# Optimization experiments

Hardware: AMD Instinct MI355X
Metric: run time of the kernel (lower is better)

The kernel has to match this reference:

```python
import jax, jax.numpy as jnp
import numpy as np

K, N, D, NCONV, E = 3, 30000, 128, 6, 480000


def _graph_conv(x, src, dst, ew, Wp, bp, Wrel, Wroot):
    # SAGE-style project=True: pre-project+relu source features
    h = jax.nn.relu(x @ Wp + bp)                    # [N, D]
    msg = ew[:, None] * h[src]                      # [E, D] gather
    agg = jax.ops.segment_sum(msg, dst, num_segments=N)
    cnt = jax.ops.segment_sum(jnp.ones_like(ew), dst, num_segments=N)
    agg = agg / jnp.maximum(cnt, 1.0)[:, None]      # mean aggregation
    return agg @ Wrel + x @ Wroot                   # GraphConv: lin_rel(agg)+lin_root(x), bias=False


def setup_inputs() -> dict:
    key = jax.random.key(0)
    ks = jax.random.split(key, 16)
    w = lambda k, s: (jax.random.normal(k, s, jnp.float32) * 0.05)
    inp = {
        "H_K_prev": jax.random.normal(ks[0], (K, N, D), jnp.float32),
        "edgelists": jax.random.randint(ks[1], (K, 2, E), 0, N, jnp.int32),
        "spec_weight": jax.random.uniform(ks[2], (K, NCONV, E), jnp.float32),
        # 6 stacked GraphConv params
        "Wp": w(ks[3], (NCONV, D, D)),
        "bp": jnp.zeros((NCONV, D), jnp.float32),
        "Wrel": w(ks[4], (NCONV, D, D)),
        "Wroot": w(ks[5], (NCONV, D, D)),
        # combine projection (7D -> 3D) and proj_linear (4D -> D)
        "W_comb": w(ks[6], ((NCONV + 1) * D, 3 * D)),
        "b_comb": jnp.zeros((3 * D,), jnp.float32),
        "W_pl": w(ks[7], (4 * D, D)),
        "b_pl": jnp.zeros((D,), jnp.float32),
        # LSTM (torch gate order i,f,g,o)
        "Wih": w(ks[8], (4 * D, D)),
        "Whh": w(ks[9], (4 * D, D)),
        "bih": jnp.zeros((4 * D,), jnp.float32),
        "bhh": jnp.zeros((4 * D,), jnp.float32),
    }
    return inp


def reference(H_K_prev, edgelists, spec_weight, Wp, bp, Wrel, Wroot,
              W_comb, b_comb, W_pl, b_pl, Wih, Whh, bih, bhh):
    outs = []
    for k in range(K):  # fixed small history loop
        Hk = H_K_prev[k]
        src, dst = edgelists[k, 0], edgelists[k, 1]
        feats = [Hk] + [
            _graph_conv(Hk, src, dst, spec_weight[k, i],
                        Wp[i], bp[i], Wrel[i], Wroot[i])
            for i in range(NCONV)
        ]
        cat = jnp.concatenate(feats, axis=1)               # [N, 7D]
        proj = jax.nn.relu(cat @ W_comb + b_comb)          # [N, 3D] (dropout=eval identity)
        outs.append(jnp.concatenate([Hk, proj], axis=1) @ W_pl + b_pl)  # [N, D]
    xs = jnp.stack(outs, 0)                                # [K, N, D] time-major

    def cell(carry, x_t):
        h, c = carry
        gates = x_t @ Wih.T + h @ Whh.T + bih + bhh        # [N, 4D]
        i, f, g, o = jnp.split(gates, 4, axis=1)
        c = jax.nn.sigmoid(f) * c + jax.nn.sigmoid(i) * jnp.tanh(g)
        h = jax.nn.sigmoid(o) * jnp.tanh(c)
        return (h, c), None

    z = jnp.zeros((N, D), xs.dtype)
    (h, _), _ = jax.lax.scan(cell, (z, z), xs)
    return jax.nn.relu(h)[None]                            # [1, N, D]
```

## Files before the change

### kernel.cpp

```cpp
#include <hip/hip_runtime.h>
#include <math.h>

constexpr int NN  = 30000;
constexpr int DIM = 128;
constexpr int KH  = 3;
constexpr int NC  = 6;
constexpr int EE  = 480000;
constexpr int NBLK3 = (3 * NN + 255) / 256;

typedef __attribute__((ext_vector_type(8))) short short8;
typedef __attribute__((ext_vector_type(4))) float f32x4;
typedef __attribute__((ext_vector_type(2))) float f32x2;

__device__ __forceinline__ unsigned short f2bf(float f) {
    union { float f; unsigned int i; } c; c.f = f;
    unsigned int u = c.i;
    return (unsigned short)((u + 0x7fffu + ((u >> 16) & 1u)) >> 16);
}
__device__ __forceinline__ float bf2f(unsigned int u) {
    union { unsigned int i; float f; } c; c.i = u << 16; return c.f;
}
__device__ __forceinline__ unsigned int packbf(float x, float y) {
    return (unsigned int)f2bf(x) | ((unsigned int)f2bf(y) << 16);
}
__device__ __forceinline__ float fsig(float x) {
    return __builtin_amdgcn_rcpf(1.f + __expf(-x));
}
__device__ __forceinline__ float ftanh(float x) {
    return 2.f * fsig(2.f * x) - 1.f;
}

template<int OUT, bool RELU>
__global__ __launch_bounds__(256) void mgemm(
    const unsigned short* __restrict__ A1, int lda1,
    const unsigned short* __restrict__ A2, int lda2, int ksplit,
    const unsigned short* __restrict__ Bt, int ldb,
    const float* __restrict__ bias,
    void* __restrict__ Cv, int ldc,
    int M, int K, int nx)
{
    __shared__ __align__(16) unsigned char smem[2 * 128 * 80];
    unsigned char* As = smem;
    unsigned char* Bs = smem + 128 * 80;

    const int nwg  = gridDim.x;
    const int orig = blockIdx.x;
    const int q = nwg >> 3, r = nwg & 7;
    const int xcd = orig & 7, idx = orig >> 3;
    const int lin = (xcd < r ? xcd * (q + 1) : r * (q + 1) + (xcd - r) * q) + idx;
    const int bx = lin % nx, by = lin / nx;

    const int tid  = threadIdx.x;
    const int lane = tid & 63;
    const int w    = tid >> 6;
    const int wm   = w >> 1, wn = w & 1;
    const int lm   = lane & 15, lg = lane >> 4;
    const int bm   = by * 128;
    const int bn   = bx * 128;

    const int srow  = tid >> 1;
    const int shalf = tid & 1;

    f32x4 acc[4][4] = {};

    int arow = bm + srow; if (arow > M - 1) arow = M - 1;
    const int brow = bn + srow;

    for (int k0 = 0; k0 < K; k0 += 32) {
        const unsigned short* Ap; int la; int kk;
        if (k0 < ksplit) { Ap = A1; la = lda1; kk = k0; }
        else             { Ap = A2; la = lda2; kk = k0 - ksplit; }
        const float4* ga = (const float4*)(Ap + (size_t)arow * la + kk + shalf * 16);
        float4 a0 = ga[0], a1 = ga[1];
        const float4* gb = (const float4*)(Bt + (size_t)brow * ldb + k0 + shalf * 16);
        float4 b0 = gb[0], b1 = gb[1];

        __syncthreads();
        *(float4*)(As + srow * 80 + shalf * 32)      = a0;
        *(float4*)(As + srow * 80 + shalf * 32 + 16) = a1;
        *(float4*)(Bs + srow * 80 + shalf * 32)      = b0;
        *(float4*)(Bs + srow * 80 + shalf * 32 + 16) = b1;
        __syncthreads();

        short8 av[4], bv[4];
        #pragma unroll
        for (int f = 0; f < 4; ++f) {
            av[f] = *(const short8*)(As + (wm * 64 + f * 16 + lm) * 80 + lg * 16);
            bv[f] = *(const short8*)(Bs + (wn * 64 + f * 16 + lm) * 80 + lg * 16);
        }
        #pragma unroll
        for (int i = 0; i < 4; ++i)
            #pragma unroll
            for (int j = 0; j < 4; ++j)
                acc[i][j] = __builtin_amdgcn_mfma_f32_16x16x32_bf16(
                    av[i], bv[j], acc[i][j], 0, 0, 0);
    }

    #pragma unroll
    for (int i = 0; i < 4; ++i) {
        int row0 = bm + wm * 64 + i * 16 + lg * 4;
        #pragma unroll
        for (int j = 0; j < 4; ++j) {
            int col = bn + wn * 64 + j * 16 + lm;
            float bb = bias[col];
            #pragma unroll
            for (int r = 0; r < 4; ++r) {
                int row = row0 + r;
                if (row < M) {
                    float v = acc[i][j][r] + bb;
                    if (RELU) v = fmaxf(v, 0.f);
                    if (OUT == 0) {
                        ((unsigned short*)Cv)[(size_t)row * ldc + col] = f2bf(v);
                    } else {
                        unsigned int pk = __builtin_amdgcn_cvt_pk_fp8_f32(v, v, 0, false);
                        ((unsigned char*)Cv)[(size_t)row * ldc + col] = (unsigned char)pk;
                    }
                }
            }
        }
    }
}

__global__ void hist3(const int* __restrict__ EL, int* __restrict__ cnt)
{
    int i = blockIdx.x * 256 + threadIdx.x;
    if (i >= 3 * EE) return;
    int g = i / EE;
    int e = i - g * EE;
    int dst = EL[(size_t)g * 2 * EE + EE + e];
    atomicAdd(&cnt[g * NN + dst], 1);
}

__global__ __launch_bounds__(256) void scan_part(const int* __restrict__ cnt,
                                                 int* __restrict__ off,
                                                 int* __restrict__ bsum, int n)
{
    int lane = threadIdx.x & 63, wid = threadIdx.x >> 6;
    int i = blockIdx.x * 256 + threadIdx.x;
    int v = (i < n) ? cnt[i] : 0;
    int x = v;
    #pragma unroll
    for (int ofs = 1; ofs < 64; ofs <<= 1) {
        int t = __shfl_up(x, ofs, 64);
        if (lane >= ofs) x += t;
    }
    __shared__ int ws[4];
    if (lane == 63) ws[wid] = x;
    __syncthreads();
    int wo = 0;
    for (int j = 0; j < wid; ++j) wo += ws[j];
    if (i < n) off[i] = wo + x - v;
    if (threadIdx.x == 255) bsum[blockIdx.x] = wo + x;
}

__global__ __launch_bounds__(512) void scan_tops(const int* __restrict__ bsum,
                                                 int* __restrict__ btop, int nb)
{
    __shared__ int buf[512];
    int v = (threadIdx.x < nb) ? bsum[threadIdx.x] : 0;
    buf[threadIdx.x] = v;
    __syncthreads();
    #pragma unroll
    for (int ofs = 1; ofs < 512; ofs <<= 1) {
        int t = (threadIdx.x >= ofs) ? buf[threadIdx.x - ofs] : 0;
        __syncthreads();
        buf[threadIdx.x] += t;
        __syncthreads();
    }
    if (threadIdx.x < nb) btop[threadIdx.x] = buf[threadIdx.x] - v;
}

__global__ __launch_bounds__(256) void scan_add(int* __restrict__ off,
                                                const int* __restrict__ btop,
                                                int* __restrict__ cursor,
                                                int n, int etot)
{
    int i = blockIdx.x * 256 + threadIdx.x;
    if (i < n) {
        int o = off[i] + btop[blockIdx.x];
        off[i] = o;
        cursor[i] = o;
    }
    if (blockIdx.x == 0 && threadIdx.x == 0) off[n] = etot;
}

__global__ void fill3(const int* __restrict__ EL, const float* __restrict__ SW,
                      int* __restrict__ cursor, int* __restrict__ csr_src,
                      uint2* __restrict__ swp)
{
    int i = blockIdx.x * 256 + threadIdx.x;
    if (i >= 3 * EE) return;
    int g = i / EE;
    int e = i - g * EE;
    const int* base = EL + (size_t)g * 2 * EE;
    int src = base[e], dst = base[EE + e];
    int pos = atomicAdd(&cursor[g * NN + dst], 1);
    csr_src[pos] = src;
    const float* sw = SW + (size_t)g * NC * EE;
    uint2 lo, hi;
    lo.x = packbf(sw[e],                   sw[(size_t)EE + e]);
    lo.y = packbf(sw[2 * (size_t)EE + e],  0.f);
    hi.x = packbf(sw[3 * (size_t)EE + e],  sw[4 * (size_t)EE + e]);
    hi.y = packbf(sw[5 * (size_t)EE + e],  0.f);
    swp[(size_t)pos * 2]     = lo;
    swp[(size_t)pos * 2 + 1] = hi;
}

__global__ __launch_bounds__(256) void gather6(
    const unsigned char* __restrict__ h8,
    const uint2* __restrict__ swp,
    const int* __restrict__ csr_src,
    const int* __restrict__ off,
    unsigned short* __restrict__ agg)
{
    int wid  = threadIdx.x >> 6;
    int lane = threadIdx.x & 63;
    int node = blockIdx.x * 2 + (wid >> 1);
    int half = wid & 1;
    if (node >= NN) return;
    int s0 = off[node], s1 = off[node + 1];
    float a0 = 0.f, a1 = 0.f, b0 = 0.f, b1 = 0.f, c0 = 0.f, c1 = 0.f;
    const size_t hofs = (size_t)half * 384 + (size_t)lane * 2;

    int e = s0;
    for (; e + 3 < s1; e += 4) {
        int sA = csr_src[e],     sB = csr_src[e + 1];
        int sC = csr_src[e + 2], sD = csr_src[e + 3];
        uint2 wA = swp[(size_t)(e    ) * 2 + half];
        uint2 wB = swp[(size_t)(e + 1) * 2 + half];
        uint2 wC = swp[(size_t)(e + 2) * 2 + half];
        uint2 wD = swp[(size_t)(e + 3) * 2 + half];
        const unsigned short* rA = (const unsigned short*)(h8 + (size_t)sA * 768 + hofs);
        const unsigned short* rB = (const unsigned short*)(h8 + (size_t)sB * 768 + hofs);
        const unsigned short* rC = (const unsigned short*)(h8 + (size_t)sC * 768 + hofs);
        const unsigned short* rD = (const unsigned short*)(h8 + (size_t)sD * 768 + hofs);
        unsigned int pA0 = rA[0], pA1 = rA[64], pA2 = rA[128];
        unsigned int pB0 = rB[0], pB1 = rB[64], pB2 = rB[128];
        unsigned int pC0 = rC[0], pC1 = rC[64], pC2 = rC[128];
        unsigned int pD0 = rD[0], pD1 = rD[64], pD2 = rD[128];

        {
            float w0 = bf2f(wA.x & 0xffffu), w1 = bf2f(wA.x >> 16), w2 = bf2f(wA.y & 0xffffu);
            f32x2 h0 = __builtin_amdgcn_cvt_pk_f32_fp8(pA0, false);
            f32x2 h1 = __builtin_amdgcn_cvt_pk_f32_fp8(pA1, false);
            f32x2 h2 = __builtin_amdgcn_cvt_pk_f32_fp8(pA2, false);
            a0 += w0 * h0.x; a1 += w0 * h0.y;
            b0 += w1 * h1.x; b1 += w1 * h1.y;
            c0 += w2 * h2.x; c1 += w2 * h2.y;
        }
        {
            float w0 = bf2f(wB.x & 0xffffu), w1 = bf2f(wB.x >> 16), w2 = bf2f(wB.y & 0xffffu);
            f32x2 h0 = __builtin_amdgcn_cvt_pk_f32_fp8(pB0, false);
            f32x2 h1 = __builtin_amdgcn_cvt_pk_f32_fp8(pB1, false);
            f32x2 h2 = __builtin_amdgcn_cvt_pk_f32_fp8(pB2, false);
            a0 += w0 * h0.x; a1 += w0 * h0.y;
            b0 += w1 * h1.x; b1 += w1 * h1.y;
            c0 += w2 * h2.x; c1 += w2 * h2.y;
        }
        {
            float w0 = bf2f(wC.x & 0xffffu), w1 = bf2f(wC.x >> 16), w2 = bf2f(wC.y & 0xffffu);
            f32x2 h0 = __builtin_amdgcn_cvt_pk_f32_fp8(pC0, false);
            f32x2 h1 = __builtin_amdgcn_cvt_pk_f32_fp8(pC1, false);
            f32x2 h2 = __builtin_amdgcn_cvt_pk_f32_fp8(pC2, false);
            a0 += w0 * h0.x; a1 += w0 * h0.y;
            b0 += w1 * h1.x; b1 += w1 * h1.y;
            c0 += w2 * h2.x; c1 += w2 * h2.y;
        }
        {
            float w0 = bf2f(wD.x & 0xffffu), w1 = bf2f(wD.x >> 16), w2 = bf2f(wD.y & 0xffffu);
            f32x2 h0 = __builtin_amdgcn_cvt_pk_f32_fp8(pD0, false);
            f32x2 h1 = __builtin_amdgcn_cvt_pk_f32_fp8(pD1, false);
            f32x2 h2 = __builtin_amdgcn_cvt_pk_f32_fp8(pD2, false);
            a0 += w0 * h0.x; a1 += w0 * h0.y;
            b0 += w1 * h1.x; b1 += w1 * h1.y;
            c0 += w2 * h2.x; c1 += w2 * h2.y;
        }
    }
    for (; e < s1; ++e) {
        int src = csr_src[e];
        uint2 wv = swp[(size_t)e * 2 + half];
        float w0 = bf2f(wv.x & 0xffffu);
        float w1 = bf2f(wv.x >> 16);
        float w2 = bf2f(wv.y & 0xffffu);
        const unsigned short* hrow = (const unsigned short*)(h8 + (size_t)src * 768 + hofs);
        unsigned int p0 = hrow[0];
        unsigned int p1 = hrow[64];
        unsigned int p2 = hrow[128];
        f32x2 h0 = __builtin_amdgcn_cvt_pk_f32_fp8(p0, false);
        f32x2 h1 = __builtin_amdgcn_cvt_pk_f32_fp8(p1, false);
        f32x2 h2 = __builtin_amdgcn_cvt_pk_f32_fp8(p2, false);
        a0 += w0 * h0.x; a1 += w0 * h0.y;
        b0 += w1 * h1.x; b1 += w1 * h1.y;
        c0 += w2 * h2.x; c1 += w2 * h2.y;
    }
    float inv = 1.f / fmaxf((float)(s1 - s0), 1.f);
    unsigned int* orow = (unsigned int*)(agg + (size_t)node * 768) + 192 * half + lane;
    orow[0]   = packbf(a0 * inv, a1 * inv);
    orow[64]  = packbf(b0 * inv, b1 * inv);
    orow[128] = packbf(c0 * inv, c1 * inv);
}

__global__ void cvt_h(const float* __restrict__ Hk, unsigned int* __restrict__ out,
                      int total)
{
    int idx = blockIdx.x * 256 + threadIdx.x;
    if (idx >= total) return;
    float2 v = ((const float2*)Hk)[idx];
    out[idx] = packbf(v.x, v.y);
}

#define SWA32(r, b) ((r) * 512 + ((b) ^ (((r) & 7) << 4)))

__global__ __launch_bounds__(512) void lstm_fused(
    const unsigned short* __restrict__ xs,
    const unsigned short* __restrict__ Wt,
    const float* __restrict__ bsum,
    float* __restrict__ outp)
{
    __shared__ __align__(16) unsigned char AL[32 * 512];

    const int tid  = threadIdx.x;
    const int lane = tid & 63;
    const int w    = tid >> 6;
    const int lm   = lane & 15, lg = lane >> 4;
    const int node0 = blockIdx.x * 32;

    float bias[4];
    #pragma unroll
    for (int g = 0; g < 4; ++g)
        bias[g] = bsum[w * 64 + g * 16 + lm];

    short8 bw[8][4];
    #pragma unroll
    for (int ks = 0; ks < 8; ++ks)
        #pragma unroll
        for (int g = 0; g < 4; ++g)
            bw[ks][g] = *(const short8*)(Wt +
                (size_t)(w * 64 + g * 16 + lm) * 256 + ks * 32 + lg * 8);

    float cst[2][4] = {};

    float4 z4 = make_float4(0.f, 0.f, 0.f, 0.f);
    {
        int r = tid >> 4, gi = tid & 15;
        *(float4*)(AL + SWA32(r, 256 + gi * 16)) = z4;
    }

    for (int t = 0; t < KH; ++t) {
        const unsigned short* xsrc = xs + (size_t)t * NN * 128;
        {
            int r = tid >> 4, gi = tid & 15;
            int gr = node0 + r; if (gr >= NN) gr = NN - 1;
            float4 v = *(const float4*)(xsrc + (size_t)gr * 128 + gi * 8);
            *(float4*)(AL + SWA32(r, gi * 16)) = v;
        }
        __syncthreads();

        f32x4 acc[2][4] = {};
        #pragma unroll
        for (int ks = 0; ks < 8; ++ks) {
            short8 av[2];
            #pragma unroll
            for (int i = 0; i < 2; ++i)
                av[i] = *(const short8*)(AL + SWA32(i * 16 + lm, ks * 64 + lg * 16));
            #pragma unroll
            for (int g = 0; g < 4; ++g)
                #pragma unroll
                for (int i = 0; i < 2; ++i)
                    acc[i][g] = __builtin_amdgcn_mfma_f32_16x16x32_bf16(
                        av[i], bw[ks][g], acc[i][g], 0, 0, 0);
        }
        __syncthreads();

        #pragma unroll
        for (int i = 0; i < 2; ++i)
            #pragma unroll
            for (int r = 0; r < 4; ++r) {
                float giv = acc[i][0][r] + bias[0];
                float gfv = acc[i][1][r] + bias[1];
                float ggv = acc[i][2][r] + bias[2];
                float gov = acc[i][3][r] + bias[3];
                float si = fsig(giv);
                float sf = fsig(gfv);
                float so = fsig(gov);
                float cv = sf * cst[i][r] + si * ftanh(ggv);
                cst[i][r] = cv;
                float hv = so * ftanh(cv);
                int row = i * 16 + lg * 4 + r;
                int d   = w * 16 + lm;
                if (t < KH - 1) {
                    *(unsigned short*)(AL + SWA32(row, 256 + 2 * d)) = f2bf(hv);
                } else if (node0 + row < NN) {
                    outp[(size_t)(node0 + row) * 128 + d] = fmaxf(hv, 0.f);
                }
            }
    }
}

__global__ __launch_bounds__(256) void wt_fold(
    const float* __restrict__ Wcomb,
    const float* __restrict__ Wroot,
    const float* __restrict__ Wrel,
    unsigned short* __restrict__ Wfull_t)
{
    __shared__ __align__(16) float As[16][68];
    __shared__ __align__(16) float Bs[16][68];
    const int tid = threadIdx.x;
    const int tx = tid & 15, ty = tid >> 4;
    const int bm = blockIdx.y * 64;
    const int bn = blockIdx.x * 64;
    const bool root = (bm < 128);
    const int i0 = root ? 0 : (bm >> 7) - 1;
    const int i1 = root ? NC : i0 + 1;
    const int mloc = bm & 127;
    const int a_m = tid >> 2, a_k = (tid & 3) * 4;
    const int b_k = tid >> 4, b_n = (tid & 15) * 4;

    float acc[4][4] = {};

    for (int i = i0; i < i1; ++i) {
        const float* A = (root ? Wroot : Wrel) + (size_t)i * 128 * 128;
        const float* B = Wcomb + (size_t)(i + 1) * 128 * 384;
        for (int k0 = 0; k0 < 128; k0 += 16) {
            float4 va = *(const float4*)(A + (size_t)(mloc + a_m) * 128 + k0 + a_k);
            float4 vb = *(const float4*)(B + (size_t)(k0 + b_k) * 384 + bn + b_n);
            __syncthreads();
            As[a_k + 0][a_m] = va.x; As[a_k + 1][a_m] = va.y;
            As[a_k + 2][a_m] = va.z; As[a_k + 3][a_m] = va.w;
            *(float4*)&Bs[b_k][b_n] = vb;
            __syncthreads();
            #pragma unroll
            for (int kk = 0; kk < 16; ++kk) {
                float4 av = *(const float4*)&As[kk][ty * 4];
                float4 bv = *(const float4*)&Bs[kk][tx * 4];
                float a[4] = {av.x, av.y, av.z, av.w};
                float b[4] = {bv.x, bv.y, bv.z, bv.w};
                #pragma unroll
                for (int ii = 0; ii < 4; ++ii)
                    #pragma unroll
                    for (int j = 0; j < 4; ++j)
                        acc[ii][j] += a[ii] * b[j];
            }
        }
    }

    #pragma unroll
    for (int ii = 0; ii < 4; ++ii) {
        int m = bm + ty * 4 + ii;
        #pragma unroll
        for (int j = 0; j < 4; ++j) {
            int n = bn + tx * 4 + j;
            float v = acc[ii][j];
            if (root) v += Wcomb[(size_t)m * 384 + n];
            Wfull_t[(size_t)n * 896 + m] = f2bf(v);
        }
    }
}

__global__ __launch_bounds__(256) void tr_cvt(
    const float* __restrict__ src, unsigned short* __restrict__ dst,
    int R, int C)
{
    __shared__ float s[32][33];
    const float* sb = src + (size_t)blockIdx.z * R * C;
    unsigned short* db = dst + (size_t)blockIdx.z * R * C;
    int r0 = blockIdx.y * 32, c0 = blockIdx.x * 32;
    int tx = threadIdx.x & 31, ty = threadIdx.x >> 5;
    #pragma unroll
    for (int q = 0; q < 4; ++q)
        s[ty + q * 8][tx] = sb[(size_t)(r0 + ty + q * 8) * C + c0 + tx];
    __syncthreads();
    #pragma unroll
    for (int q = 0; q < 4; ++q)
        db[(size_t)(c0 + ty + q * 8) * R + r0 + tx] = f2bf(s[tx][ty + q * 8]);
}

__global__ void wt_lstm(const float* __restrict__ Wih, const float* __restrict__ Whh,
                        const float* __restrict__ bih, const float* __restrict__ bhh,
                        unsigned short* __restrict__ Wt, float* __restrict__ bsum)
{
    int idx = blockIdx.x * 256 + threadIdx.x;
    if (idx < 512) {
        int w = idx >> 6, rem = idx & 63, g = rem >> 4, d16 = rem & 15;
        int n = g * 128 + w * 16 + d16;
        bsum[idx] = bih[n] + bhh[n];
    }
    if (idx >= 512 * 256) return;
    int k = idx & 255, np = idx >> 8;
    int w = np >> 6, rem = np & 63, g = rem >> 4, d16 = rem & 15;
    int n = g * 128 + w * 16 + d16;
    Wt[idx] = f2bf(k < 128 ? Wih[(size_t)n * DIM + k]
                           : Whh[(size_t)n * DIM + (k - 128)]);
}

extern "C" void kernel_launch(void* const* d_in, const int* in_sizes, int n_in,
                              void* d_out, int out_size, void* d_ws, size_t ws_size,
                              hipStream_t stream)
{
    const float* H     = (const float*)d_in[0];
    const int*   EL    = (const int*)  d_in[1];
    const float* SW    = (const float*)d_in[2];
    const float* Wp    = (const float*)d_in[3];
    const float* bp    = (const float*)d_in[4];
    const float* Wrel  = (const float*)d_in[5];
    const float* Wroot = (const float*)d_in[6];
    const float* Wcomb = (const float*)d_in[7];
    const float* bcomb = (const float*)d_in[8];
    const float* Wpl   = (const float*)d_in[9];
    const float* bpl   = (const float*)d_in[10];
    const float* Wih   = (const float*)d_in[11];
    const float* Whh   = (const float*)d_in[12];
    const float* bih   = (const float*)d_in[13];
    const float* bhh   = (const float*)d_in[14];

    char* wp = (char*)d_ws;
    auto alloc = [&](size_t b) {
        char* p = wp; wp += (b + 255) & ~(size_t)255; return p;
    };
    unsigned short* Hbf  = (unsigned short*)alloc((size_t)3 * NN * 128 * 2);
    unsigned char*  h8   = (unsigned char*) alloc((size_t)NN * 768);
    unsigned short* agg  = (unsigned short*)alloc((size_t)NN * 768 * 2);
    unsigned short* proj = (unsigned short*)alloc((size_t)NN * 384 * 2);
    unsigned short* xs   = (unsigned short*)alloc((size_t)KH * NN * 128 * 2);
    int* cnt     = (int*)alloc((size_t)3 * NN * 4);
    int* off     = (int*)alloc((size_t)(3 * NN + 1) * 4);
    int* cursor  = (int*)alloc((size_t)3 * NN * 4);
    int* bsum    = (int*)alloc((size_t)NBLK3 * 4);
    int* btop    = (int*)alloc((size_t)NBLK3 * 4);
    int* csr_src = (int*)alloc((size_t)3 * EE * 4);
    uint2* swp   = (uint2*)alloc((size_t)3 * EE * 16);
    unsigned short* Wp_t     = (unsigned short*)alloc((size_t)768 * 128 * 2);
    unsigned short* Wfull_t  = (unsigned short*)alloc((size_t)384 * 896 * 2);
    unsigned short* Wpl_t    = (unsigned short*)alloc((size_t)128 * 512 * 2);
    unsigned short* WihWhh_t = (unsigned short*)alloc((size_t)512 * 256 * 2);
    float* bias_lstm         = (float*)alloc(512 * 4);

    tr_cvt<<<dim3(4, 4, 6), 256, 0, stream>>>(Wp, Wp_t, 128, 128);
    wt_fold<<<dim3(6, 14), 256, 0, stream>>>(Wcomb, Wroot, Wrel, Wfull_t);
    tr_cvt<<<dim3(4, 16, 1), 256, 0, stream>>>(Wpl, Wpl_t, 512, 128);
    wt_lstm<<<(512 * 256 + 255) / 256, 256, 0, stream>>>(Wih, Whh, bih, bhh,
                                                         WihWhh_t, bias_lstm);

    hipMemsetAsync(cnt, 0, (size_t)3 * NN * 4, stream);
    hist3<<<(3 * EE + 255) / 256, 256, 0, stream>>>(EL, cnt);
    scan_part<<<NBLK3, 256, 0, stream>>>(cnt, off, bsum, 3 * NN);
    scan_tops<<<1, 512, 0, stream>>>(bsum, btop, NBLK3);
    scan_add<<<NBLK3, 256, 0, stream>>>(off, btop, cursor, 3 * NN, 3 * EE);
    fill3<<<(3 * EE + 255) / 256, 256, 0, stream>>>(EL, SW, cursor, csr_src, swp);

    cvt_h<<<(3 * NN * 64 + 255) / 256, 256, 0, stream>>>(H, (unsigned int*)Hbf,
                                                         3 * NN * 64);

    const int MB = (NN + 127) / 128;

    for (int k = 0; k < KH; ++k) {
        const unsigned short* Hbk = Hbf + (size_t)k * NN * 128;

        mgemm<1, true><<<6 * MB, 256, 0, stream>>>(
            Hbk, 128, (const unsigned short*)nullptr, 0, 128,
            Wp_t, 128, bp, h8, 768, NN, 128, 6);

        gather6<<<NN / 2, 256, 0, stream>>>(h8, swp, csr_src, off + k * NN, agg);

        mgemm<0, true><<<3 * MB, 256, 0, stream>>>(
            Hbk, 128, agg, 768, 128,
            Wfull_t, 896, bcomb, proj, 384, NN, 896, 3);

        mgemm<0, false><<<1 * MB, 256, 0, stream>>>(
            Hbk, 128, proj, 384, 128,
            Wpl_t, 512, bpl, xs + (size_t)k * NN * 128, 128, NN, 512, 1);
    }

    lstm_fused<<<(NN + 31) / 32, 512, 0, stream>>>(xs, WihWhh_t, bias_lstm,
                                                   (float*)d_out);
}
```

Before: 738.3 us.

## Use direct global-to-LDS loads in GEMM and pack edge records into one struct

```diff
diff --git a/kernel.cpp b/kernel.cpp
--- a/kernel.cpp
+++ b/kernel.cpp
@@ -29,6 +29,11 @@
 __device__ __forceinline__ float ftanh(float x) {
     return 2.f * fsig(2.f * x) - 1.f;
 }
+
+#define GLD16(gp, lp)                                                        \
+    __builtin_amdgcn_global_load_lds(                                        \
+        (const __attribute__((address_space(1))) unsigned int*)(gp),         \
+        (__attribute__((address_space(3))) unsigned int*)(lp), 16, 0, 0)
 
 template<int OUT, bool RELU>
 __global__ __launch_bounds__(256) void mgemm(
@@ -39,9 +44,9 @@
     void* __restrict__ Cv, int ldc,
     int M, int K, int nx)
 {
-    __shared__ __align__(16) unsigned char smem[2 * 128 * 80];
+    __shared__ __align__(16) unsigned char smem[2 * 8192];
     unsigned char* As = smem;
-    unsigned char* Bs = smem + 128 * 80;
+    unsigned char* Bs = smem + 8192;
 
     const int nwg  = gridDim.x;
     const int orig = blockIdx.x;
@@ -58,35 +63,35 @@
     const int bm   = by * 128;
     const int bn   = bx * 128;
 
-    const int srow  = tid >> 1;
-    const int shalf = tid & 1;
-
     f32x4 acc[4][4] = {};
 
-    int arow = bm + srow; if (arow > M - 1) arow = M - 1;
-    const int brow = bn + srow;
+    int arow0 = bm + lane;      if (arow0 > M - 1) arow0 = M - 1;
+    int arow1 = bm + 64 + lane; if (arow1 > M - 1) arow1 = M - 1;
+    const int brow0 = bn + lane;
+    const int brow1 = bn + 64 + lane;
+
+    unsigned char* Adst0 = As + w * 2048;
+    unsigned char* Adst1 = As + w * 2048 + 1024;
+    unsigned char* Bdst0 = Bs + w * 2048;
+    unsigned char* Bdst1 = Bs + w * 2048 + 1024;
 
     for (int k0 = 0; k0 < K; k0 += 32) {
         const unsigned short* Ap; int la; int kk;
         if (k0 < ksplit) { Ap = A1; la = lda1; kk = k0; }
         else             { Ap = A2; la = lda2; kk = k0 - ksplit; }
-        const float4* ga = (const float4*)(Ap + (size_t)arow * la + kk + shalf * 16);
-        float4 a0 = ga[0], a1 = ga[1];
-        const float4* gb = (const float4*)(Bt + (size_t)brow * ldb + k0 + shalf * 16);
-        float4 b0 = gb[0], b1 = gb[1];
 
         __syncthreads();
-        *(float4*)(As + srow * 80 + shalf * 32)      = a0;
-        *(float4*)(As + srow * 80 + shalf * 32 + 16) = a1;
-        *(float4*)(Bs + srow * 80 + shalf * 32)      = b0;
-        *(float4*)(Bs + srow * 80 + shalf * 32 + 16) = b1;
+        GLD16(Ap + (size_t)arow0 * la + kk + w * 8, Adst0);
+        GLD16(Ap + (size_t)arow1 * la + kk + w * 8, Adst1);
+        GLD16(Bt + (size_t)brow0 * ldb + k0 + w * 8, Bdst0);
+        GLD16(Bt + (size_t)brow1 * ldb + k0 + w * 8, Bdst1);
         __syncthreads();
 
         short8 av[4], bv[4];
         #pragma unroll
         for (int f = 0; f < 4; ++f) {
-            av[f] = *(const short8*)(As + (wm * 64 + f * 16 + lm) * 80 + lg * 16);
-            bv[f] = *(const short8*)(Bs + (wn * 64 + f * 16 + lm) * 80 + lg * 16);
+            av[f] = *(const short8*)(As + lg * 2048 + (wm * 64 + f * 16 + lm) * 16);
+            bv[f] = *(const short8*)(Bs + lg * 2048 + (wn * 64 + f * 16 + lm) * 16);
         }
         #pragma unroll
         for (int i = 0; i < 4; ++i)
@@ -104,10 +109,10 @@
             int col = bn + wn * 64 + j * 16 + lm;
             float bb = bias[col];
             #pragma unroll
-            for (int r = 0; r < 4; ++r) {
-                int row = row0 + r;
+            for (int r2 = 0; r2 < 4; ++r2) {
+                int row = row0 + r2;
                 if (row < M) {
-                    float v = acc[i][j][r] + bb;
+                    float v = acc[i][j][r2] + bb;
                     if (RELU) v = fmaxf(v, 0.f);
                     if (OUT == 0) {
                         ((unsigned short*)Cv)[(size_t)row * ldc + col] = f2bf(v);
@@ -185,8 +190,7 @@
 }
 
 __global__ void fill3(const int* __restrict__ EL, const float* __restrict__ SW,
-                      int* __restrict__ cursor, int* __restrict__ csr_src,
-                      uint2* __restrict__ swp)
+                      int* __restrict__ cursor, uint4* __restrict__ rec)
 {
     int i = blockIdx.x * 256 + threadIdx.x;
     if (i >= 3 * EE) return;
@@ -195,21 +199,28 @@
     const int* base = EL + (size_t)g * 2 * EE;
     int src = base[e], dst = base[EE + e];
     int pos = atomicAdd(&cursor[g * NN + dst], 1);
-    csr_src[pos] = src;
     const float* sw = SW + (size_t)g * NC * EE;
-    uint2 lo, hi;
-    lo.x = packbf(sw[e],                   sw[(size_t)EE + e]);
-    lo.y = packbf(sw[2 * (size_t)EE + e],  0.f);
-    hi.x = packbf(sw[3 * (size_t)EE + e],  sw[4 * (size_t)EE + e]);
-    hi.y = packbf(sw[5 * (size_t)EE + e],  0.f);
-    swp[(size_t)pos * 2]     = lo;
-    swp[(size_t)pos * 2 + 1] = hi;
+    uint4 rv;
+    rv.x = (unsigned int)src;
+    rv.y = packbf(sw[e],                  sw[(size_t)EE + e]);
+    rv.z = packbf(sw[2 * (size_t)EE + e], sw[3 * (size_t)EE + e]);
+    rv.w = packbf(sw[4 * (size_t)EE + e], sw[5 * (size_t)EE + e]);
+    rec[pos] = rv;
+}
+
+__device__ __forceinline__ void wunpack(uint4 r, int half,
+                                        float& w0, float& w1, float& w2)
+{
+    if (half == 0) {
+        w0 = bf2f(r.y & 0xffffu); w1 = bf2f(r.y >> 16); w2 = bf2f(r.z & 0xffffu);
+    } else {
+        w0 = bf2f(r.z >> 16); w1 = bf2f(r.w & 0xffffu); w2 = bf2f(r.w >> 16);
+    }
 }
 
 __global__ __launch_bounds__(256) void gather6(
     const unsigned char* __restrict__ h8,
-    const uint2* __restrict__ swp,
-    const int* __restrict__ csr_src,
+    const uint4* __restrict__ rec,
     const int* __restrict__ off,
     unsigned short* __restrict__ agg)
 {
@@ -224,23 +235,19 @@
 
     int e = s0;
     for (; e + 3 < s1; e += 4) {
-        int sA = csr_src[e],     sB = csr_src[e + 1];
-        int sC = csr_src[e + 2], sD = csr_src[e + 3];
-        uint2 wA = swp[(size_t)(e    ) * 2 + half];
-        uint2 wB = swp[(size_t)(e + 1) * 2 + half];
-        uint2 wC = swp[(size_t)(e + 2) * 2 + half];
-        uint2 wD = swp[(size_t)(e + 3) * 2 + half];
-        const unsigned short* rA = (const unsigned short*)(h8 + (size_t)sA * 768 + hofs);
-        const unsigned short* rB = (const unsigned short*)(h8 + (size_t)sB * 768 + hofs);
-        const unsigned short* rC = (const unsigned short*)(h8 + (size_t)sC * 768 + hofs);
-        const unsigned short* rD = (const unsigned short*)(h8 + (size_t)sD * 768 + hofs);
-        unsigned int pA0 = rA[0], pA1 = rA[64], pA2 = rA[128];
-        unsigned int pB0 = rB[0], pB1 = rB[64], pB2 = rB[128];
-        unsigned int pC0 = rC[0], pC1 = rC[64], pC2 = rC[128];
-        unsigned int pD0 = rD[0], pD1 = rD[64], pD2 = rD[128];
-
+        uint4 rA = rec[e], rB = rec[e + 1], rC = rec[e + 2], rD = rec[e + 3];
+        const unsigned short* pA = (const unsigned short*)(h8 + (size_t)rA.x * 768 + hofs);
+        const unsigned short* pB = (const unsigned short*)(h8 + (size_t)rB.x * 768 + hofs);
+        const unsigned short* pC = (const unsigned short*)(h8 + (size_t)rC.x * 768 + hofs);
+        const unsigned short* pD = (const unsigned short*)(h8 + (size_t)rD.x * 768 + hofs);
+        unsigned int pA0 = pA[0], pA1 = pA[64], pA2 = pA[128];
+        unsigned int pB0 = pB[0], pB1 = pB[64], pB2 = pB[128];
+        unsigned int pC0 = pC[0], pC1 = pC[64], pC2 = pC[128];
+        unsigned int pD0 = pD[0], pD1 = pD[64], pD2 = pD[128];
+
+        float w0, w1, w2;
+        wunpack(rA, half, w0, w1, w2);
         {
-            float w0 = bf2f(wA.x & 0xffffu), w1 = bf2f(wA.x >> 16), w2 = bf2f(wA.y & 0xffffu);
             f32x2 h0 = __builtin_amdgcn_cvt_pk_f32_fp8(pA0, false);
             f32x2 h1 = __builtin_amdgcn_cvt_pk_f32_fp8(pA1, false);
             f32x2 h2 = __builtin_amdgcn_cvt_pk_f32_fp8(pA2, false);
@@ -248,8 +255,8 @@
             b0 += w1 * h1.x; b1 += w1 * h1.y;
             c0 += w2 * h2.x; c1 += w2 * h2.y;
         }
+        wunpack(rB, half, w0, w1, w2);
         {
-            float w0 = bf2f(wB.x & 0xffffu), w1 = bf2f(wB.x >> 16), w2 = bf2f(wB.y & 0xffffu);
             f32x2 h0 = __builtin_amdgcn_cvt_pk_f32_fp8(pB0, false);
             f32x2 h1 = __builtin_amdgcn_cvt_pk_f32_fp8(pB1, false);
             f32x2 h2 = __builtin_amdgcn_cvt_pk_f32_fp8(pB2, false);
@@ -257,8 +264,8 @@
             b0 += w1 * h1.x; b1 += w1 * h1.y;
             c0 += w2 * h2.x; c1 += w2 * h2.y;
         }
+        wunpack(rC, half, w0, w1, w2);
         {
-            float w0 = bf2f(wC.x & 0xffffu), w1 = bf2f(wC.x >> 16), w2 = bf2f(wC.y & 0xffffu);
             f32x2 h0 = __builtin_amdgcn_cvt_pk_f32_fp8(pC0, false);
             f32x2 h1 = __builtin_amdgcn_cvt_pk_f32_fp8(pC1, false);
             f32x2 h2 = __builtin_amdgcn_cvt_pk_f32_fp8(pC2, false);
@@ -266,8 +273,8 @@
             b0 += w1 * h1.x; b1 += w1 * h1.y;
             c0 += w2 * h2.x; c1 += w2 * h2.y;
         }
+        wunpack(rD, half, w0, w1, w2);
         {
-            float w0 = bf2f(wD.x & 0xffffu), w1 = bf2f(wD.x >> 16), w2 = bf2f(wD.y & 0xffffu);
             f32x2 h0 = __builtin_amdgcn_cvt_pk_f32_fp8(pD0, false);
             f32x2 h1 = __builtin_amdgcn_cvt_pk_f32_fp8(pD1, false);
             f32x2 h2 = __builtin_amdgcn_cvt_pk_f32_fp8(pD2, false);
@@ -277,12 +284,10 @@
         }
     }
     for (; e < s1; ++e) {
-        int src = csr_src[e];
-        uint2 wv = swp[(size_t)e * 2 + half];
-        float w0 = bf2f(wv.x & 0xffffu);
-        float w1 = bf2f(wv.x >> 16);
-        float w2 = bf2f(wv.y & 0xffffu);
-        const unsigned short* hrow = (const unsigned short*)(h8 + (size_t)src * 768 + hofs);
+        uint4 r = rec[e];
+        float w0, w1, w2;
+        wunpack(r, half, w0, w1, w2);
+        const unsigned short* hrow = (const unsigned short*)(h8 + (size_t)r.x * 768 + hofs);
         unsigned int p0 = hrow[0];
         unsigned int p1 = hrow[64];
         unsigned int p2 = hrow[128];
@@ -527,8 +532,7 @@
     int* cursor  = (int*)alloc((size_t)3 * NN * 4);
     int* bsum    = (int*)alloc((size_t)NBLK3 * 4);
     int* btop    = (int*)alloc((size_t)NBLK3 * 4);
-    int* csr_src = (int*)alloc((size_t)3 * EE * 4);
-    uint2* swp   = (uint2*)alloc((size_t)3 * EE * 16);
+    uint4* rec   = (uint4*)alloc((size_t)3 * EE * 16);
     unsigned short* Wp_t     = (unsigned short*)alloc((size_t)768 * 128 * 2);
     unsigned short* Wfull_t  = (unsigned short*)alloc((size_t)384 * 896 * 2);
     unsigned short* Wpl_t    = (unsigned short*)alloc((size_t)128 * 512 * 2);
@@ -546,7 +550,7 @@
     scan_part<<<NBLK3, 256, 0, stream>>>(cnt, off, bsum, 3 * NN);
     scan_tops<<<1, 512, 0, stream>>>(bsum, btop, NBLK3);
     scan_add<<<NBLK3, 256, 0, stream>>>(off, btop, cursor, 3 * NN, 3 * EE);
-    fill3<<<(3 * EE + 255) / 256, 256, 0, stream>>>(EL, SW, cursor, csr_src, swp);
+    fill3<<<(3 * EE + 255) / 256, 256, 0, stream>>>(EL, SW, cursor, rec);
 
     cvt_h<<<(3 * NN * 64 + 255) / 256, 256, 0, stream>>>(H, (unsigned int*)Hbf,
                                                          3 * NN * 64);
@@ -560,7 +564,7 @@
             Hbk, 128, (const unsigned short*)nullptr, 0, 128,
             Wp_t, 128, bp, h8, 768, NN, 128, 6);
 
-        gather6<<<NN / 2, 256, 0, stream>>>(h8, swp, csr_src, off + k * NN, agg);
+        gather6<<<NN / 2, 256, 0, stream>>>(h8, rec, off + k * NN, agg);
 
         mgemm<0, true><<<3 * MB, 256, 0, stream>>>(
             Hbk, 128, agg, 768, 128,
```

Measured after the change: 795.7 us. 1.08x slower.
